# Kernel tuning notes

Measured on AMD Instinct MI355X. Metric: run time of the kernel, lower is better.

## Reference

```python
import jax, jax.numpy as jnp
import numpy as np


def setup_inputs() -> dict:
    key = jax.random.key(0)
    ks = jax.random.split(key, 7)
    N, D, H1, H2, M = 16384, 2048, 512, 32, 2048
    return {
        "x": jax.random.normal(ks[0], (N, D), dtype=jnp.float32),
        "W1": jax.random.normal(ks[1], (H1, D), dtype=jnp.float32) * (1.0 / np.sqrt(D)),
        "b1": jax.random.normal(ks[2], (H1,), dtype=jnp.float32) * 0.01,
        "W2": jax.random.normal(ks[3], (H2, H1), dtype=jnp.float32) * (1.0 / np.sqrt(H1)),
        "b2": jax.random.normal(ks[4], (H2,), dtype=jnp.float32) * 0.01,
        "a_memory": jax.random.normal(ks[5], (M, H2), dtype=jnp.float32),
        "n_memory": jax.random.normal(ks[6], (M, H2), dtype=jnp.float32),
    }


def reference(x, W1, b1, W2, b2, a_memory, n_memory):
    # MLP per forward(): linear -> relu -> (dropout p=0) -> linear -> (dropout p=0)
    h = jax.nn.relu(x @ W1.T + b1)          # [N, 512]
    feat = h @ W2.T + b2                     # [N, 32] (no ReLU in forward path)
    inv_d = 1.0 / feat.shape[1]
    # caption_score(mem, f) = max_j mean(mem_j * f) = max_j (mem_j . f) / 32
    a_score = jnp.max(feat @ a_memory.T, axis=1) * inv_d  # [N]
    n_score = jnp.max(feat @ n_memory.T, axis=1) * inv_d  # [N]
    return jax.nn.sigmoid(a_score - n_score)
```

## Files before the change

kernel.cpp:

```cpp
#include <hip/hip_runtime.h>
#include <hip/hip_bf16.h>

typedef __attribute__((ext_vector_type(8))) __bf16 bf16x8;
typedef __attribute__((ext_vector_type(4))) float f32x4;

#define NROWS 16384
#define DIM   2048
#define NH1   512
#define NH2   32
#define MMEM  2048
#define BK    32
#define NT    (DIM / BK)

#define W1O ((size_t)0)
#define W2O ((size_t)2097152)
#define AMO ((size_t)2129920)
#define NMO ((size_t)2260992)
#define HO  ((size_t)2392064)

__device__ __forceinline__ f32x4 mfma16(bf16x8 a, bf16x8 b, f32x4 c) {
    return __builtin_amdgcn_mfma_f32_16x16x32_bf16(a, b, c, 0, 0, 0);
}

__device__ __forceinline__ void gload_lds16(const void* g, void* l) {
    __builtin_amdgcn_global_load_lds(
        (const __attribute__((address_space(1))) void*)g,
        (__attribute__((address_space(3))) void*)l, 16, 0, 0);
}

__device__ __forceinline__ bf16x8 cvt8(f32x4 a, f32x4 b) {
    bf16x8 o;
    o[0] = (__bf16)a[0]; o[1] = (__bf16)a[1]; o[2] = (__bf16)a[2]; o[3] = (__bf16)a[3];
    o[4] = (__bf16)b[0]; o[5] = (__bf16)b[1]; o[6] = (__bf16)b[2]; o[7] = (__bf16)b[3];
    return o;
}

struct bf4 { __bf16 a, b, c, d; };

__global__ void cvt_all_kernel(const float* __restrict__ w1f, __bf16* __restrict__ w1b,
                               const float* __restrict__ w2f, __bf16* __restrict__ w2b,
                               const float* __restrict__ amf, __bf16* __restrict__ amb,
                               const float* __restrict__ nmf, __bf16* __restrict__ nmb) {
    const int g = blockIdx.x * blockDim.x + threadIdx.x;
    const int T = gridDim.x * blockDim.x;
    for (int i = g; i < (NH1 * DIM) / 4; i += T) {
        const float4 v = *reinterpret_cast<const float4*>(w1f + i * 4);
        *reinterpret_cast<bf4*>(w1b + i * 4) = { (__bf16)v.x, (__bf16)v.y, (__bf16)v.z, (__bf16)v.w };
    }
    for (int i = g; i < (NH2 * NH1) / 4; i += T) {
        const float4 v = *reinterpret_cast<const float4*>(w2f + i * 4);
        *reinterpret_cast<bf4*>(w2b + i * 4) = { (__bf16)v.x, (__bf16)v.y, (__bf16)v.z, (__bf16)v.w };
    }
    for (int i = g; i < (MMEM * NH2) / 4; i += T) {
        const float4 v = *reinterpret_cast<const float4*>(amf + i * 4);
        *reinterpret_cast<bf4*>(amb + i * 4) = { (__bf16)v.x, (__bf16)v.y, (__bf16)v.z, (__bf16)v.w };
    }
    for (int i = g; i < (MMEM * NH2) / 4; i += T) {
        const float4 v = *reinterpret_cast<const float4*>(nmf + i * 4);
        *reinterpret_cast<bf4*>(nmb + i * 4) = { (__bf16)v.x, (__bf16)v.y, (__bf16)v.z, (__bf16)v.w };
    }
}

__global__ __launch_bounds__(256, 2) void gemm1_kernel(
    const float*  __restrict__ Xf,
    const __bf16* __restrict__ W1,
    const float*  __restrict__ b1,
    __bf16* __restrict__ Hout)
{
    __shared__ float  As[3][128 * BK];
    __shared__ __bf16 Bs[3][128 * BK];
    const int tid  = threadIdx.x;
    const int lane = tid & 63;
    const int wave = tid >> 6;
    const int b = blockIdx.x;
    const int orig = (b & 7) * 64 + (b >> 3);
    const int bn = orig & 3;
    const int bm = orig >> 2;
    const size_t brow = (size_t)bm * 128;
    const int bcol = bn * 128;
    const int wr = wave >> 1, wc = wave & 1;

    f32x4 acc[4][4];
#pragma unroll
    for (int m = 0; m < 4; ++m)
#pragma unroll
        for (int n = 0; n < 4; ++n) acc[m][n] = (f32x4){0.f, 0.f, 0.f, 0.f};

    const int aRowT = tid >> 3;
    const int cA    = (tid & 7) ^ (aRowT & 7);
    const float* aSrcBase = Xf + (brow + aRowT) * (size_t)DIM + cA * 4;
    const int bRowT = tid >> 2;
    const int cB    = (tid & 3) ^ (bRowT & 3);
    const __bf16* bSrcBase = W1 + (size_t)(bcol + bRowT) * DIM + cB * 8;

#define STAGE(T, BI)                                                          \
    {                                                                         \
        const int k0_ = (T) * BK;                                             \
        _Pragma("unroll")                                                     \
        for (int q = 0; q < 4; ++q)                                           \
            gload_lds16(aSrcBase + (size_t)q * 32 * DIM + k0_,                \
                        (char*)As[BI] + q * 4096 + tid * 16);                 \
        _Pragma("unroll")                                                     \
        for (int q = 0; q < 2; ++q)                                           \
            gload_lds16(bSrcBase + (size_t)q * 64 * DIM + k0_,                \
                        (char*)Bs[BI] + q * 4096 + tid * 16);                 \
    }

    const int l15 = lane & 15;
    const int kc  = lane >> 4;
    const int l7  = lane & 7;
    const int rABase = wr * 64 + l15;
    const int rBBase = wc * 64 + l15;
    const int aSlot0 = ((2 * kc)     ^ l7) << 4;
    const int aSlot1 = ((2 * kc + 1) ^ l7) << 4;
    const int bSlot  = (kc ^ (lane & 3)) << 4;

#define COMPUTE(BI)                                                           \
    {                                                                         \
        const char* Ac = (const char*)As[BI];                                 \
        const char* Bc = (const char*)Bs[BI];                                 \
        bf16x8 av[4], bv[4];                                                  \
        _Pragma("unroll")                                                     \
        for (int m = 0; m < 4; ++m) {                                         \
            const int rowB = (rABase + m * 16) * 128;                         \
            f32x4 lo = *(const f32x4*)(Ac + rowB + aSlot0);                   \
            f32x4 hi = *(const f32x4*)(Ac + rowB + aSlot1);                   \
            av[m] = cvt8(lo, hi);                                             \
        }                                                                     \
        _Pragma("unroll")                                                     \
        for (int n = 0; n < 4; ++n)                                           \
            bv[n] = *(const bf16x8*)(Bc + (rBBase + n * 16) * 64 + bSlot);    \
        __builtin_amdgcn_s_setprio(1);                                        \
        _Pragma("unroll")                                                     \
        for (int m = 0; m < 4; ++m)                                           \
            _Pragma("unroll")                                                 \
            for (int n = 0; n < 4; ++n)                                       \
                acc[m][n] = mfma16(av[m], bv[n], acc[m][n]);                  \
        __builtin_amdgcn_s_setprio(0);                                        \
    }

    STAGE(0, 0);
    STAGE(1, 1);

    for (int t = 0; t < NT - 2; ++t) {
        const int bi = t % 3;
        asm volatile("s_waitcnt vmcnt(6)" ::: "memory");
        __builtin_amdgcn_s_barrier();
        __builtin_amdgcn_sched_barrier(0);
        COMPUTE(bi);
        __builtin_amdgcn_sched_barrier(0);
        const int bnx = (t + 2) % 3;
        STAGE(t + 2, bnx);
    }
    {
        asm volatile("s_waitcnt vmcnt(6)" ::: "memory");
        __builtin_amdgcn_s_barrier();
        __builtin_amdgcn_sched_barrier(0);
        COMPUTE((NT - 2) % 3);
        asm volatile("s_waitcnt vmcnt(0)" ::: "memory");
        __builtin_amdgcn_s_barrier();
        __builtin_amdgcn_sched_barrier(0);
        COMPUTE((NT - 1) % 3);
    }
#undef STAGE
#undef COMPUTE

#pragma unroll
    for (int n = 0; n < 4; ++n) {
        const int gcol = bcol + wc * 64 + n * 16 + l15;
        const float bias = b1[gcol];
#pragma unroll
        for (int m = 0; m < 4; ++m) {
            const size_t grow0 = brow + wr * 64 + m * 16 + kc * 4;
#pragma unroll
            for (int r = 0; r < 4; ++r) {
                float v = acc[m][n][r] + bias;
                v = v > 0.f ? v : 0.f;
                Hout[(grow0 + r) * NH1 + gcol] = (__bf16)v;
            }
        }
    }
}

__global__ __launch_bounds__(512) void tail_kernel(
    const __bf16* __restrict__ Hin,
    const __bf16* __restrict__ W2b,
    const float*  __restrict__ b2,
    const __bf16* __restrict__ Am,
    const __bf16* __restrict__ Nm,
    float* __restrict__ out)
{
    __shared__ __bf16 featLds[64 * 32];
    __shared__ float aMaxLds[2][64];
    __shared__ float nMaxLds[2][64];
    const int tid  = threadIdx.x;
    const int lane = tid & 63;
    const int wave = tid >> 6;
    const int rowBase = blockIdx.x * 64;
    const int l15 = lane & 15;
    const int kc  = lane >> 4;
    const int rgrp  = (wave & 3) * 16;
    const int jHalf = wave >> 2;

    if (wave < 4) {
        f32x4 acc0 = {0.f,0.f,0.f,0.f}, acc1 = {0.f,0.f,0.f,0.f};
        const size_t hrow = (size_t)(rowBase + rgrp + l15) * NH1;
#pragma unroll
        for (int kk = 0; kk < 16; ++kk) {
            bf16x8 a  = *(const bf16x8*)(Hin + hrow + kk * 32 + kc * 8);
            bf16x8 w0 = *(const bf16x8*)(W2b + (size_t)l15 * NH1 + kk * 32 + kc * 8);
            bf16x8 w1 = *(const bf16x8*)(W2b + (size_t)(16 + l15) * NH1 + kk * 32 + kc * 8);
            acc0 = mfma16(a, w0, acc0);
            acc1 = mfma16(a, w1, acc1);
        }
        const float bias0 = b2[l15], bias1 = b2[16 + l15];
#pragma unroll
        for (int r = 0; r < 4; ++r) {
            const int lr = rgrp + kc * 4 + r;
            featLds[lr * 32 + l15]      = (__bf16)(acc0[r] + bias0);
            featLds[lr * 32 + 16 + l15] = (__bf16)(acc1[r] + bias1);
        }
    }
    __syncthreads();

    const bf16x8 af = *(const bf16x8*)&featLds[(rgrp + l15) * 32 + kc * 8];

    float rmaxA[4], rmaxN[4];
#pragma unroll
    for (int r = 0; r < 4; ++r) { rmaxA[r] = -1e30f; rmaxN[r] = -1e30f; }
    const f32x4 zero = {0.f,0.f,0.f,0.f};
    const int jBase = jHalf * (MMEM / 2);
#pragma unroll 2
    for (int jt = 0; jt < (MMEM / 2) / 16; jt += 4) {
        bf16x8 ba[4], bb[4];
#pragma unroll
        for (int u = 0; u < 4; ++u) {
            const size_t off = (size_t)(jBase + (jt + u) * 16 + l15) * NH2 + kc * 8;
            ba[u] = *(const bf16x8*)(Am + off);
            bb[u] = *(const bf16x8*)(Nm + off);
        }
#pragma unroll
        for (int u = 0; u < 4; ++u) {
            f32x4 sa = mfma16(af, ba[u], zero);
            f32x4 sn = mfma16(af, bb[u], zero);
#pragma unroll
            for (int r = 0; r < 4; ++r) {
                rmaxA[r] = fmaxf(rmaxA[r], sa[r]);
                rmaxN[r] = fmaxf(rmaxN[r], sn[r]);
            }
        }
    }
#pragma unroll
    for (int off = 1; off < 16; off <<= 1) {
#pragma unroll
        for (int r = 0; r < 4; ++r) {
            rmaxA[r] = fmaxf(rmaxA[r], __shfl_xor(rmaxA[r], off, 64));
            rmaxN[r] = fmaxf(rmaxN[r], __shfl_xor(rmaxN[r], off, 64));
        }
    }
    if (l15 == 0) {
#pragma unroll
        for (int r = 0; r < 4; ++r) {
            const int row = rgrp + kc * 4 + r;
            aMaxLds[jHalf][row] = rmaxA[r];
            nMaxLds[jHalf][row] = rmaxN[r];
        }
    }
    __syncthreads();
    if (tid < 64) {
        const float ma = fmaxf(aMaxLds[0][tid], aMaxLds[1][tid]);
        const float mn = fmaxf(nMaxLds[0][tid], nMaxLds[1][tid]);
        const float d = (ma - mn) * (1.0f / 32.0f);
        out[rowBase + tid] = 1.0f / (1.0f + __expf(-d));
    }
}

extern "C" void kernel_launch(void* const* d_in, const int* in_sizes, int n_in,
                              void* d_out, int out_size, void* d_ws, size_t ws_size,
                              hipStream_t stream) {
    (void)in_sizes; (void)n_in; (void)out_size; (void)ws_size;
    const float* x  = (const float*)d_in[0];
    const float* W1 = (const float*)d_in[1];
    const float* b1 = (const float*)d_in[2];
    const float* W2 = (const float*)d_in[3];
    const float* b2 = (const float*)d_in[4];
    const float* am = (const float*)d_in[5];
    const float* nm = (const float*)d_in[6];
    float* out = (float*)d_out;
    char* ws = (char*)d_ws;
    __bf16* w1b = (__bf16*)(ws + W1O);
    __bf16* w2b = (__bf16*)(ws + W2O);
    __bf16* amb = (__bf16*)(ws + AMO);
    __bf16* nmb = (__bf16*)(ws + NMO);
    __bf16* hb  = (__bf16*)(ws + HO);

    cvt_all_kernel<<<dim3(512), dim3(256), 0, stream>>>(W1, w1b, W2, w2b, am, amb, nm, nmb);
    gemm1_kernel<<<dim3((NROWS / 128) * (NH1 / 128)), dim3(256), 0, stream>>>(x, w1b, b1, hb);
    tail_kernel<<<dim3(NROWS / 64), dim3(512), 0, stream>>>(hb, w2b, b2, amb, nmb, out);
}
```

Measured before the change: 81.67 us.

## Deepen W1 prefetch pipeline and issue loads before compute in GEMM1

```diff
diff --git a/kernel.cpp b/kernel.cpp
--- a/kernel.cpp
+++ b/kernel.cpp
@@ -68,7 +68,7 @@
     __bf16* __restrict__ Hout)
 {
     __shared__ float  As[3][128 * BK];
-    __shared__ __bf16 Bs[3][128 * BK];
+    __shared__ __bf16 Bs[4][128 * BK];
     const int tid  = threadIdx.x;
     const int lane = tid & 63;
     const int wave = tid >> 6;
@@ -90,16 +90,20 @@
     const int cA    = (tid & 7) ^ (aRowT & 7);
     const float* aSrcBase = Xf + (brow + aRowT) * (size_t)DIM + cA * 4;
     const int bRowT = tid >> 2;
-    const int cB    = (tid & 3) ^ (bRowT & 3);
+    const int cB    = (tid & 3) ^ ((tid >> 3) & 3);
     const __bf16* bSrcBase = W1 + (size_t)(bcol + bRowT) * DIM + cB * 8;
 
-#define STAGE(T, BI)                                                          \
+#define STAGE_A(T, BI)                                                        \
     {                                                                         \
         const int k0_ = (T) * BK;                                             \
         _Pragma("unroll")                                                     \
         for (int q = 0; q < 4; ++q)                                           \
             gload_lds16(aSrcBase + (size_t)q * 32 * DIM + k0_,                \
                         (char*)As[BI] + q * 4096 + tid * 16);                 \
+    }
+#define STAGE_B(T, BI)                                                        \
+    {                                                                         \
+        const int k0_ = (T) * BK;                                             \
         _Pragma("unroll")                                                     \
         for (int q = 0; q < 2; ++q)                                           \
             gload_lds16(bSrcBase + (size_t)q * 64 * DIM + k0_,                \
@@ -113,11 +117,11 @@
     const int rBBase = wc * 64 + l15;
     const int aSlot0 = ((2 * kc)     ^ l7) << 4;
     const int aSlot1 = ((2 * kc + 1) ^ l7) << 4;
-    const int bSlot  = (kc ^ (lane & 3)) << 4;
-
-#define COMPUTE(BI)                                                           \
+    const int bSlot  = (kc ^ ((l15 >> 1) & 3)) << 4;
+
+#define COMPUTE(AI, BI)                                                       \
     {                                                                         \
-        const char* Ac = (const char*)As[BI];                                 \
+        const char* Ac = (const char*)As[AI];                                 \
         const char* Bc = (const char*)Bs[BI];                                 \
         bf16x8 av[4], bv[4];                                                  \
         _Pragma("unroll")                                                     \
@@ -139,30 +143,29 @@
         __builtin_amdgcn_s_setprio(0);                                        \
     }
 
-    STAGE(0, 0);
-    STAGE(1, 1);
-
-    for (int t = 0; t < NT - 2; ++t) {
-        const int bi = t % 3;
-        asm volatile("s_waitcnt vmcnt(6)" ::: "memory");
+    STAGE_A(0, 0);
+    STAGE_B(0, 0);
+    STAGE_A(1, 1);
+    STAGE_B(1, 1);
+    STAGE_B(2, 2);
+
+    int ia = 0;
+    int i2 = 2;
+    for (int t = 0; t < NT; ++t) {
+        asm volatile("s_waitcnt vmcnt(8)" ::: "memory");
         __builtin_amdgcn_s_barrier();
         __builtin_amdgcn_sched_barrier(0);
-        COMPUTE(bi);
+        const int tA = (t + 2 < NT) ? (t + 2) : (NT - 1);
+        const int tB = (t + 3 < NT) ? (t + 3) : (NT - 1);
+        STAGE_A(tA, i2);
+        STAGE_B(tB, (t + 3) & 3);
         __builtin_amdgcn_sched_barrier(0);
-        const int bnx = (t + 2) % 3;
-        STAGE(t + 2, bnx);
-    }
-    {
-        asm volatile("s_waitcnt vmcnt(6)" ::: "memory");
-        __builtin_amdgcn_s_barrier();
-        __builtin_amdgcn_sched_barrier(0);
-        COMPUTE((NT - 2) % 3);
-        asm volatile("s_waitcnt vmcnt(0)" ::: "memory");
-        __builtin_amdgcn_s_barrier();
-        __builtin_amdgcn_sched_barrier(0);
-        COMPUTE((NT - 1) % 3);
-    }
-#undef STAGE
+        COMPUTE(ia, t & 3);
+        ia = (ia == 2) ? 0 : ia + 1;
+        i2 = (i2 == 2) ? 0 : i2 + 1;
+    }
+#undef STAGE_A
+#undef STAGE_B
 #undef COMPUTE
 
 #pragma unroll
```

Result: slower. 91.73 us (+12.3%).

## Shrink GEMM1 tile to 64x128 with double buffering and higher occupancy

Applied to the files above, without the earlier changes.

```diff
diff --git a/kernel.cpp b/kernel.cpp
--- a/kernel.cpp
+++ b/kernel.cpp
@@ -61,28 +61,28 @@
     }
 }
 
-__global__ __launch_bounds__(256, 2) void gemm1_kernel(
+__global__ __launch_bounds__(256, 4) void gemm1_kernel(
     const float*  __restrict__ Xf,
     const __bf16* __restrict__ W1,
     const float*  __restrict__ b1,
     __bf16* __restrict__ Hout)
 {
-    __shared__ float  As[3][128 * BK];
-    __shared__ __bf16 Bs[3][128 * BK];
+    __shared__ float  Af[2][64 * BK];
+    __shared__ __bf16 Bs[2][128 * BK];
     const int tid  = threadIdx.x;
     const int lane = tid & 63;
     const int wave = tid >> 6;
     const int b = blockIdx.x;
-    const int orig = (b & 7) * 64 + (b >> 3);
+    const int orig = (b & 7) * 128 + (b >> 3);
     const int bn = orig & 3;
     const int bm = orig >> 2;
-    const size_t brow = (size_t)bm * 128;
+    const size_t brow = (size_t)bm * 64;
     const int bcol = bn * 128;
     const int wr = wave >> 1, wc = wave & 1;
 
-    f32x4 acc[4][4];
-#pragma unroll
-    for (int m = 0; m < 4; ++m)
+    f32x4 acc[2][4];
+#pragma unroll
+    for (int m = 0; m < 2; ++m)
 #pragma unroll
         for (int n = 0; n < 4; ++n) acc[m][n] = (f32x4){0.f, 0.f, 0.f, 0.f};
 
@@ -90,16 +90,16 @@
     const int cA    = (tid & 7) ^ (aRowT & 7);
     const float* aSrcBase = Xf + (brow + aRowT) * (size_t)DIM + cA * 4;
     const int bRowT = tid >> 2;
-    const int cB    = (tid & 3) ^ (bRowT & 3);
+    const int cB    = (tid & 3) ^ ((tid >> 3) & 3);
     const __bf16* bSrcBase = W1 + (size_t)(bcol + bRowT) * DIM + cB * 8;
 
 #define STAGE(T, BI)                                                          \
     {                                                                         \
         const int k0_ = (T) * BK;                                             \
         _Pragma("unroll")                                                     \
-        for (int q = 0; q < 4; ++q)                                           \
+        for (int q = 0; q < 2; ++q)                                           \
             gload_lds16(aSrcBase + (size_t)q * 32 * DIM + k0_,                \
-                        (char*)As[BI] + q * 4096 + tid * 16);                 \
+                        (char*)Af[BI] + q * 4096 + tid * 16);                 \
         _Pragma("unroll")                                                     \
         for (int q = 0; q < 2; ++q)                                           \
             gload_lds16(bSrcBase + (size_t)q * 64 * DIM + k0_,                \
@@ -109,19 +109,19 @@
     const int l15 = lane & 15;
     const int kc  = lane >> 4;
     const int l7  = lane & 7;
-    const int rABase = wr * 64 + l15;
+    const int rABase = wr * 32 + l15;
     const int rBBase = wc * 64 + l15;
     const int aSlot0 = ((2 * kc)     ^ l7) << 4;
     const int aSlot1 = ((2 * kc + 1) ^ l7) << 4;
-    const int bSlot  = (kc ^ (lane & 3)) << 4;
+    const int bSlot  = (kc ^ ((l15 >> 1) & 3)) << 4;
 
 #define COMPUTE(BI)                                                           \
     {                                                                         \
-        const char* Ac = (const char*)As[BI];                                 \
+        const char* Ac = (const char*)Af[BI];                                 \
         const char* Bc = (const char*)Bs[BI];                                 \
-        bf16x8 av[4], bv[4];                                                  \
-        _Pragma("unroll")                                                     \
-        for (int m = 0; m < 4; ++m) {                                         \
+        bf16x8 av[2], bv[4];                                                  \
+        _Pragma("unroll")                                                     \
+        for (int m = 0; m < 2; ++m) {                                         \
             const int rowB = (rABase + m * 16) * 128;                         \
             f32x4 lo = *(const f32x4*)(Ac + rowB + aSlot0);                   \
             f32x4 hi = *(const f32x4*)(Ac + rowB + aSlot1);                   \
@@ -130,37 +130,20 @@
         _Pragma("unroll")                                                     \
         for (int n = 0; n < 4; ++n)                                           \
             bv[n] = *(const bf16x8*)(Bc + (rBBase + n * 16) * 64 + bSlot);    \
-        __builtin_amdgcn_s_setprio(1);                                        \
-        _Pragma("unroll")                                                     \
-        for (int m = 0; m < 4; ++m)                                           \
+        _Pragma("unroll")                                                     \
+        for (int m = 0; m < 2; ++m)                                           \
             _Pragma("unroll")                                                 \
             for (int n = 0; n < 4; ++n)                                       \
                 acc[m][n] = mfma16(av[m], bv[n], acc[m][n]);                  \
-        __builtin_amdgcn_s_setprio(0);                                        \
     }
 
     STAGE(0, 0);
-    STAGE(1, 1);
-
-    for (int t = 0; t < NT - 2; ++t) {
-        const int bi = t % 3;
-        asm volatile("s_waitcnt vmcnt(6)" ::: "memory");
-        __builtin_amdgcn_s_barrier();
-        __builtin_amdgcn_sched_barrier(0);
-        COMPUTE(bi);
-        __builtin_amdgcn_sched_barrier(0);
-        const int bnx = (t + 2) % 3;
-        STAGE(t + 2, bnx);
-    }
-    {
-        asm volatile("s_waitcnt vmcnt(6)" ::: "memory");
-        __builtin_amdgcn_s_barrier();
-        __builtin_amdgcn_sched_barrier(0);
-        COMPUTE((NT - 2) % 3);
-        asm volatile("s_waitcnt vmcnt(0)" ::: "memory");
-        __builtin_amdgcn_s_barrier();
-        __builtin_amdgcn_sched_barrier(0);
-        COMPUTE((NT - 1) % 3);
+    __syncthreads();
+
+    for (int t = 0; t < NT; ++t) {
+        if (t + 1 < NT) STAGE(t + 1, (t + 1) & 1);
+        COMPUTE(t & 1);
+        __syncthreads();
     }
 #undef STAGE
 #undef COMPUTE
@@ -170,8 +153,8 @@
         const int gcol = bcol + wc * 64 + n * 16 + l15;
         const float bias = b1[gcol];
 #pragma unroll
-        for (int m = 0; m < 4; ++m) {
-            const size_t grow0 = brow + wr * 64 + m * 16 + kc * 4;
+        for (int m = 0; m < 2; ++m) {
+            const size_t grow0 = brow + wr * 32 + m * 16 + kc * 4;
 #pragma unroll
             for (int r = 0; r < 4; ++r) {
                 float v = acc[m][n][r] + bias;
@@ -295,6 +278,6 @@
     __bf16* hb  = (__bf16*)(ws + HO);
 
     cvt_all_kernel<<<dim3(512), dim3(256), 0, stream>>>(W1, w1b, W2, w2b, am, amb, nm, nmb);
-    gemm1_kernel<<<dim3((NROWS / 128) * (NH1 / 128)), dim3(256), 0, stream>>>(x, w1b, b1, hb);
+    gemm1_kernel<<<dim3((NROWS / 64) * (NH1 / 128)), dim3(256), 0, stream>>>(x, w1b, b1, hb);
     tail_kernel<<<dim3(NROWS / 64), dim3(512), 0, stream>>>(hb, w2b, b2, amb, nmb, out);
 }
```

Result: slower. 91.66 us (+12.2%).
